# Kernel optimization log

Hardware: AMD Instinct MI355X
Metric: run time of the kernel (lower is better)

## Reference

```python
import jax, jax.numpy as jnp
import numpy as np

B, T, E, NH, NLEV = 16, 2048, 1024, 16, 12
HD = E // NH


def _level_matrix(length):
    # Vectorized version of get_level_index_weak (base=2): levels[t, s] for s < t.
    tt, ss = np.meshgrid(np.arange(length), np.arange(length), indexing='ij')
    t = tt.copy(); s = ss.copy()
    lev = np.zeros((length, length), dtype=np.int32)
    active = tt > ss
    while active.any():
        l = np.floor(np.log2(np.maximum(t, 1))).astype(np.int64)
        v = (1 << l)
        done = active & (s < v)
        lev[done] = (l[done] + 1).astype(np.int32)
        cont = active & ~done
        t = np.where(cont, t - v, t)
        s = np.where(cont, s - v, s)
        active = cont
    return lev  # lev[t,t] = 0 (diagonal uses level 0)


def setup_inputs() -> dict:
    key = jax.random.key(0)
    ks = jax.random.split(key, 12)
    s = 0.02
    inp = {
        'x': jax.random.normal(ks[0], (B, T, E), jnp.float32),
        'Wq': jax.random.normal(ks[1], (E, E), jnp.float32) * s,
        'bq': jnp.zeros((E,), jnp.float32),
        'Wk': jax.random.normal(ks[2], (E, E), jnp.float32) * s,
        'bk': jnp.zeros((E,), jnp.float32),
        'Wv': jax.random.normal(ks[3], (E, E), jnp.float32) * s,
        'bv': jnp.zeros((E,), jnp.float32),
        'A_log': jax.random.normal(ks[4], (T, NH), jnp.float32),
        'A_bias': jnp.zeros((T, NH), jnp.float32),
        'L': jax.random.normal(ks[5], (T, NH, NLEV), jnp.float32),
        'L_bias': jnp.zeros((T, NH, NLEV), jnp.float32),
        'Wo': jax.random.normal(ks[6], (E, E), jnp.float32) * s,
        'bo': jnp.zeros((E,), jnp.float32),
        'levels': jnp.asarray(_level_matrix(T)),
    }
    return inp


def reference(x, Wq, bq, Wk, bk, Wv, bv, A_log, A_bias, L, L_bias, Wo, bo, levels):
    Bn, Tn, En = x.shape
    NHh = A_log.shape[1]
    HDd = En // NHh
    # q/k projections exist in the original forward but are never used by the
    # hierarchical attention; keep only v (q/k are dead code -> omitted).
    v = (x @ Wv.T + bv).reshape(Bn, Tn, NHh, HDd).transpose(0, 2, 1, 3)  # [B,H,T,D]

    # Decay factors: prod(A[s+1:t+1]) == exp(cumsum(logA)[t] - cumsum(logA)[s]).
    A = jax.nn.sigmoid(A_log + A_bias)            # [T, H]
    cs = jnp.cumsum(jnp.log(A), axis=0)           # [T, H]
    decay = jnp.exp(cs[:, None, :] - cs[None, :, :])  # [t, s, H]; diag == 1

    # Hierarchical level weights: G[t, s, h] = (L + L_bias)[t, h, levels[t, s]].
    Le = L + L_bias                               # [T, H, NLEV]
    G = Le[jnp.arange(Tn)[:, None], :, levels]    # [t, s, H]

    causal = jnp.tril(jnp.ones((Tn, Tn), dtype=bool))[:, :, None]
    Hm = jnp.where(causal, G * decay, jnp.zeros((), x.dtype))  # [t, s, H]

    # Original softmaxes the full row (upper triangle is 0, not -inf) -> keep that.
    attn = jax.nn.softmax(Hm, axis=1)             # over source dim s
    out = jnp.einsum('tsh,bhsd->bhtd', attn, v)   # [B,H,T,D]
    out = out.transpose(0, 2, 1, 3).reshape(Bn, Tn, En)
    return out @ Wo.T + bo
```

## Files before the change

### kernel.cpp

```cpp
#include <hip/hip_runtime.h>
#include <stdint.h>

static constexpr int Bn = 16, Tn = 2048, En = 1024, NHn = 16, HDn = 64, NLEVn = 12;

typedef __attribute__((ext_vector_type(8))) short short8;
typedef __attribute__((ext_vector_type(4))) float floatx4;

__device__ __forceinline__ unsigned short f2bf(float f) {
  unsigned int u = __float_as_uint(f);
  u += 0x7fffu + ((u >> 16) & 1u);
  return (unsigned short)(u >> 16);
}
__device__ __forceinline__ float bf2f(unsigned short s) {
  return __uint_as_float(((unsigned int)s) << 16);
}

__device__ __forceinline__ void async16(const unsigned short* g, unsigned short* l) {
  __builtin_amdgcn_global_load_lds(
      (const __attribute__((address_space(1))) unsigned int*)g,
      (__attribute__((address_space(3))) unsigned int*)l, 16, 0, 0);
}

__global__ void k_cvt(const float* __restrict__ in, unsigned short* __restrict__ out, int n4) {
  int i = blockIdx.x * 256 + threadIdx.x;
  if (i < n4) {
    float4 v = ((const float4*)in)[i];
    ushort4 o;
    o.x = f2bf(v.x); o.y = f2bf(v.y); o.z = f2bf(v.z); o.w = f2bf(v.w);
    ((ushort4*)out)[i] = o;
  }
}

__global__ void k_scan(const float* __restrict__ A_log, const float* __restrict__ A_bias,
                       float* __restrict__ cs) {
  int h = blockIdx.x;
  int tid = threadIdx.x;
  __shared__ float part[256];
  float loc[8];
  float run = 0.f;
#pragma unroll
  for (int j = 0; j < 8; j++) {
    int t = tid * 8 + j;
    float x = A_log[t * NHn + h] + A_bias[t * NHn + h];
    float ls = -log1pf(__expf(-x));
    run += ls;
    loc[j] = run;
  }
  part[tid] = run;
  __syncthreads();
  for (int d = 1; d < 256; d <<= 1) {
    float v = (tid >= d) ? part[tid - d] : 0.f;
    __syncthreads();
    part[tid] += v;
    __syncthreads();
  }
  float off = (tid > 0) ? part[tid - 1] : 0.f;
#pragma unroll
  for (int j = 0; j < 8; j++) cs[(tid * 8 + j) * NHn + h] = loc[j] + off;
}

__global__ void k_weights(const float* __restrict__ L, const float* __restrict__ Lb,
                          const int* __restrict__ levels, const float* __restrict__ cs,
                          unsigned short* __restrict__ P, float* __restrict__ denom) {
  int t = blockIdx.x;
  int tid = threadIdx.x;
  __shared__ float Lrow[NHn * NLEVn];
  __shared__ float cst[NHn];
  __shared__ float dsum[NHn];
  if (tid < NHn * NLEVn) Lrow[tid] = L[t * NHn * NLEVn + tid] + Lb[t * NHn * NLEVn + tid];
  if (tid < NHn) { cst[tid] = cs[t * NHn + tid]; dsum[tid] = 0.f; }
  __syncthreads();
  float acc[NHn];
#pragma unroll
  for (int h = 0; h < NHn; h++) acc[h] = 0.f;
  for (int s = tid; s < Tn; s += 256) {
    int lev = levels[(size_t)t * Tn + s];
    bool causal = (s <= t);
    float csr[NHn];
    const float4* c4 = (const float4*)(cs + s * NHn);
#pragma unroll
    for (int q = 0; q < 4; q++) {
      float4 v = c4[q];
      csr[q * 4 + 0] = v.x; csr[q * 4 + 1] = v.y; csr[q * 4 + 2] = v.z; csr[q * 4 + 3] = v.w;
    }
#pragma unroll
    for (int h = 0; h < NHn; h++) {
      float w = 1.f;
      if (causal) {
        float dec = __expf(cst[h] - csr[h]);
        w = __expf(Lrow[h * NLEVn + lev] * dec);
      }
      unsigned short pb = f2bf(w);
      acc[h] += bf2f(pb);
      P[((size_t)h * Tn + t) * Tn + s] = pb;
    }
  }
  int lane = tid & 63;
#pragma unroll
  for (int h = 0; h < NHn; h++) {
    float v = acc[h];
    for (int o = 32; o > 0; o >>= 1) v += __shfl_down(v, o, 64);
    if (lane == 0) atomicAdd(&dsum[h], v);
  }
  __syncthreads();
  if (tid < NHn) denom[(size_t)tid * Tn + t] = dsum[tid];
}

__global__ __launch_bounds__(512)
void k_gemm_v(const unsigned short* __restrict__ A, const unsigned short* __restrict__ Bm,
              const float* __restrict__ bias, unsigned short* __restrict__ vt) {
  __shared__ unsigned short smem[24576];
  unsigned short* As = smem;
  unsigned short* Bs = smem + 16384;
  const int K = 1024;
  int tid = threadIdx.x;
  int wave = tid >> 6, lane = tid & 63;
  int wm = wave >> 1, wn = wave & 1;

  int flat = blockIdx.y * 8 + blockIdx.x;
  int xcd = flat & 7, slot = flat >> 3;
  int strip = xcd * 16 + (slot >> 3);
  int nt = slot & 7;
  int bm = strip * 256, bn = nt * 128;

  floatx4 zero4 = {0.f, 0.f, 0.f, 0.f};
  floatx4 acc[4][4];
#pragma unroll
  for (int i = 0; i < 4; i++)
#pragma unroll
    for (int j = 0; j < 4; j++) acc[i][j] = zero4;

  for (int k0 = 0; k0 < K; k0 += 64) {
    __syncthreads();
#pragma unroll
    for (int j = 0; j < 4; j++) {
      int f = j * 512 + tid;
      int r = f >> 3, c = f & 7;
      int cg = c ^ (r & 7);
      async16(&A[(size_t)(bm + r) * K + k0 + cg * 8], &As[f * 8]);
    }
#pragma unroll
    for (int j = 0; j < 2; j++) {
      int f = j * 512 + tid;
      int r = f >> 3, c = f & 7;
      int cg = c ^ (r & 7);
      async16(&Bm[(size_t)(bn + r) * K + k0 + cg * 8], &Bs[f * 8]);
    }
    __syncthreads();
#pragma unroll
    for (int kk = 0; kk < 2; kk++) {
      short8 af[4], bfr[4];
      int cgk = kk * 4 + (lane >> 4);
#pragma unroll
      for (int i = 0; i < 4; i++) {
        int m = wm * 64 + i * 16 + (lane & 15);
        af[i] = *(const short8*)&As[m * 64 + ((cgk ^ (m & 7)) * 8)];
        int n = wn * 64 + i * 16 + (lane & 15);
        bfr[i] = *(const short8*)&Bs[n * 64 + ((cgk ^ (n & 7)) * 8)];
      }
#pragma unroll
      for (int i = 0; i < 4; i++)
#pragma unroll
        for (int j = 0; j < 4; j++)
          acc[i][j] = __builtin_amdgcn_mfma_f32_16x16x32_bf16(af[i], bfr[j], acc[i][j], 0, 0, 0);
    }
  }

  int b = bm >> 11, t0 = bm & 2047;
  unsigned short* Ct = smem;
  const int S = 264;
#pragma unroll 1
  for (int pass = 0; pass < 2; pass++) {
    __syncthreads();
    if (wn == pass) {
#pragma unroll
      for (int i = 0; i < 4; i++) {
#pragma unroll
        for (int j = 0; j < 4; j++) {
          int colL = j * 16 + (lane & 15);
          float bia = bias[bn + pass * 64 + colL];
          int rowb = wm * 64 + i * 16 + (lane >> 4) * 4;
          ushort4 p;
          p.x = f2bf(acc[i][j][0] + bia);
          p.y = f2bf(acc[i][j][1] + bia);
          p.z = f2bf(acc[i][j][2] + bia);
          p.w = f2bf(acc[i][j][3] + bia);
          *(ushort4*)&Ct[colL * S + rowb] = p;
        }
      }
    }
    __syncthreads();
#pragma unroll
    for (int cc = 0; cc < 4; cc++) {
      int colL = wave * 8 + cc * 2 + (lane >> 5);
      int gc = bn + pass * 64 + colL;
      int h = gc >> 6, d = gc & 63;
      int tt = (lane & 31) * 8;
      short8 v = *(const short8*)&Ct[colL * S + tt];
      *(short8*)&vt[((size_t)((h * Bn + b) * HDn + d)) * Tn + t0 + tt] = v;
    }
  }
}


#define STAGE_A(kt, half, buf)                                                   \
  {                                                                              \
    _Pragma("unroll")                                                            \
    for (int j_ = 0; j_ < 2; j_++) {                                             \
      int f_ = j_ * 512 + tid;                                                   \
      int r_ = f_ >> 3, c_ = f_ & 7;                                             \
      int cg_ = c_ ^ (r_ & 7);                                                   \
      async16(&Ap[(size_t)(bm + (half) * 128 + r_) * K + (kt) * 64 + cg_ * 8],   \
              &smem[(buf) * 32768 + ((half) * 128 + r_) * 64 + c_ * 8]);         \
    }                                                                            \
  }

#define STAGE_B(kt, half, buf)                                                   \
  {                                                                              \
    _Pragma("unroll")                                                            \
    for (int j_ = 0; j_ < 2; j_++) {                                             \
      int f_ = j_ * 512 + tid;                                                   \
      int r_ = f_ >> 3, c_ = f_ & 7;                                             \
      int cg_ = c_ ^ (r_ & 7);                                                   \
      async16(&Bp[(size_t)(bn + (half) * 128 + r_) * K + (kt) * 64 + cg_ * 8],   \
              &smem[(buf) * 32768 + 16384 + ((half) * 128 + r_) * 64 + c_ * 8]); \
    }                                                                            \
  }

#define LOAD_A(buf, Mh)                                                          \
  {                                                                              \
    _Pragma("unroll")                                                            \
    for (int ii_ = 0; ii_ < 4; ii_++) {                                          \
      int m_ = (Mh) * 128 + wm * 64 + ii_ * 16 + (lane & 15);                    \
      _Pragma("unroll")                                                          \
      for (int kk_ = 0; kk_ < 2; kk_++) {                                        \
        int cgk_ = kk_ * 4 + (lane >> 4);                                        \
        aR[ii_][kk_] =                                                           \
            *(const short8*)&smem[(buf) * 32768 + m_ * 64 + ((cgk_ ^ (m_ & 7)) * 8)]; \
      }                                                                          \
    }                                                                            \
  }

#define LOAD_B(buf, Nh)                                                          \
  {                                                                              \
    _Pragma("unroll")                                                            \
    for (int jj_ = 0; jj_ < 2; jj_++) {                                          \
      int n_ = (Nh) * 128 + wn * 32 + jj_ * 16 + (lane & 15);                    \
      _Pragma("unroll")                                                          \
      for (int kk_ = 0; kk_ < 2; kk_++) {                                        \
        int cgk_ = kk_ * 4 + (lane >> 4);                                        \
        bR[jj_][kk_] = *(const short8*)&smem[(buf) * 32768 + 16384 + n_ * 64 +   \
                                             ((cgk_ ^ (n_ & 7)) * 8)];           \
      }                                                                          \
    }                                                                            \
  }

#define MFMA16(Mh, Nh)                                                           \
  {                                                                              \
    __builtin_amdgcn_s_setprio(1);                                               \
    _Pragma("unroll")                                                            \
    for (int kk_ = 0; kk_ < 2; kk_++)                                            \
      _Pragma("unroll")                                                          \
      for (int ii_ = 0; ii_ < 4; ii_++)                                          \
        _Pragma("unroll")                                                        \
        for (int jj_ = 0; jj_ < 2; jj_++)                                        \
          acc[(Mh) * 4 + ii_][(Nh) * 2 + jj_] = __builtin_amdgcn_mfma_f32_16x16x32_bf16( \
              aR[ii_][kk_], bR[jj_][kk_], acc[(Mh) * 4 + ii_][(Nh) * 2 + jj_], 0, 0, 0); \
    __builtin_amdgcn_s_setprio(0);                                               \
  }

#define WAIT4 asm volatile("s_waitcnt vmcnt(4)" ::: "memory")
#define LGKM8 asm volatile("s_waitcnt lgkmcnt(8)" ::: "memory")
#define BAR                                                                      \
  {                                                                              \
    asm volatile("" ::: "memory");                                               \
    __builtin_amdgcn_s_barrier();                                                \
    asm volatile("" ::: "memory");                                               \
  }

#define KTILE_BODY(buf, nbuf, tn)                                                \
  {                                                                              \
                                        \
    LOAD_A(buf, 0);                                                              \
    LOAD_B(buf, 0);                                                              \
    STAGE_A(tn, 0, nbuf);                                                        \
    LGKM8;                                                                       \
    WAIT4; BAR;                                                                  \
    MFMA16(0, 0);                                                                \
    BAR;                                                                         \
                                        \
    LOAD_B(buf, 1);                                                              \
    STAGE_B(tn, 0, nbuf);                                                        \
    WAIT4; BAR;                                                                  \
    MFMA16(0, 1);                                                                \
    BAR;                                                                         \
                                        \
    LOAD_A(buf, 1);                                                              \
    STAGE_B(tn, 1, nbuf);                                                        \
    WAIT4; BAR;                                                                  \
    MFMA16(1, 1);                                                                \
    BAR;                                                                         \
                           \
    LOAD_B(buf, 0);                                                              \
    STAGE_A(tn, 1, nbuf);                                                        \
    WAIT4; BAR;                                                                  \
    MFMA16(1, 0);                                                                \
    BAR;                                                                         \
  }

__global__ __launch_bounds__(512, 2)
void k_gemm_attn(const unsigned short* __restrict__ P, const unsigned short* __restrict__ vt,
                 const float* __restrict__ denom, unsigned short* __restrict__ outp) {
  __shared__ unsigned short smem[65536];
  const int K = Tn;
  int tid = threadIdx.x;
  int wave = tid >> 6, lane = tid & 63;
  int wm = wave >> 2, wn = wave & 3;

  int flat = blockIdx.y * 8 + blockIdx.x;
  int wg = (flat & 7) * 64 + (flat >> 3);
  int h = wg >> 5;
  int mt = (wg >> 2) & 7, nt = wg & 3;
  int bm = mt * 256, bn = nt * 256;

  const unsigned short* Ap = P + (size_t)h * Tn * Tn;
  const unsigned short* Bp = vt + (size_t)h * (Bn * HDn) * Tn;

  floatx4 zero4 = {0.f, 0.f, 0.f, 0.f};
  floatx4 acc[8][4];
#pragma unroll
  for (int i = 0; i < 8; i++)
#pragma unroll
    for (int j = 0; j < 4; j++) acc[i][j] = zero4;

  short8 aR[4][2], bR[2][2];

  STAGE_A(0, 0, 0);
  STAGE_B(0, 0, 0);
  STAGE_B(0, 1, 0);
  STAGE_A(0, 1, 0);
  WAIT4; BAR;

  const int nk = K / 64;
  for (int t = 0; t < nk; t++) {
    int buf = t & 1, nbuf = buf ^ 1;
    int tn = (t < nk - 1) ? t + 1 : nk - 1;
    KTILE_BODY(buf, nbuf, tn);
  }
  asm volatile("s_waitcnt vmcnt(0)" ::: "memory");

#pragma unroll
  for (int i = 0; i < 8; i++) {
    int rb = bm + (i >> 2) * 128 + wm * 64 + (i & 3) * 16 + (lane >> 4) * 4;
#pragma unroll
    for (int r = 0; r < 4; r++) {
      int row = rb + r;
      float sc = 1.f / denom[(size_t)h * Tn + row];
#pragma unroll
      for (int j = 0; j < 4; j++) {
        int col = bn + (j >> 1) * 128 + wn * 32 + (j & 1) * 16 + (lane & 15);
        int b = col >> 6, d = col & 63;
        outp[((size_t)(b * Tn + row)) * En + h * HDn + d] = f2bf(acc[i][j][r] * sc);
      }
    }
  }
}

__global__ __launch_bounds__(512, 2)
void k_gemm_out(const unsigned short* __restrict__ A, const unsigned short* __restrict__ Bm,
                const float* __restrict__ bias, float* __restrict__ out) {
  __shared__ unsigned short smem[65536];
  const int K = 1024, N = 1024;
  int tid = threadIdx.x;
  int wave = tid >> 6, lane = tid & 63;
  int wm = wave >> 2, wn = wave & 3;

  int flat = blockIdx.y * 8 + blockIdx.x;
  int wg = (flat & 7) * 64 + (flat >> 3);
  int mt = wg >> 2, nt = wg & 3;
  int bm = mt * 256, bn = nt * 256;

  const unsigned short* Ap = A;
  const unsigned short* Bp = Bm;

  floatx4 zero4 = {0.f, 0.f, 0.f, 0.f};
  floatx4 acc[8][4];
#pragma unroll
  for (int i = 0; i < 8; i++)
#pragma unroll
    for (int j = 0; j < 4; j++) acc[i][j] = zero4;

  short8 aR[4][2], bR[2][2];

  STAGE_A(0, 0, 0);
  STAGE_B(0, 0, 0);
  STAGE_B(0, 1, 0);
  STAGE_A(0, 1, 0);
  WAIT4; BAR;

  const int nk = K / 64;
  for (int t = 0; t < nk; t++) {
    int buf = t & 1, nbuf = buf ^ 1;
    int tn = (t < nk - 1) ? t + 1 : nk - 1;
    KTILE_BODY(buf, nbuf, tn);
  }
  asm volatile("s_waitcnt vmcnt(0)" ::: "memory");

#pragma unroll
  for (int i = 0; i < 8; i++) {
    int rb = bm + (i >> 2) * 128 + wm * 64 + (i & 3) * 16 + (lane >> 4) * 4;
#pragma unroll
    for (int r = 0; r < 4; r++) {
      int row = rb + r;
#pragma unroll
      for (int j = 0; j < 4; j++) {
        int col = bn + (j >> 1) * 128 + wn * 32 + (j & 1) * 16 + (lane & 15);
        out[(size_t)row * N + col] = acc[i][j][r] + bias[col];
      }
    }
  }
}

extern "C" void kernel_launch(void* const* d_in, const int* in_sizes, int n_in,
                              void* d_out, int out_size, void* d_ws, size_t ws_size,
                              hipStream_t stream) {
  const float* x      = (const float*)d_in[0];
  const float* Wv     = (const float*)d_in[5];
  const float* bv     = (const float*)d_in[6];
  const float* A_log  = (const float*)d_in[7];
  const float* A_bias = (const float*)d_in[8];
  const float* L      = (const float*)d_in[9];
  const float* Lb     = (const float*)d_in[10];
  const float* Wo     = (const float*)d_in[11];
  const float* bo     = (const float*)d_in[12];
  const int* levels   = (const int*)d_in[13];
  float* out = (float*)d_out;

  char* ws = (char*)d_ws;
  float* cs            = (float*)(ws + 0);
  float* denom         = (float*)(ws + 131072);
  unsigned short* Wvb  = (unsigned short*)(ws + 262144);
  unsigned short* Wob  = (unsigned short*)(ws + 2359296);
  unsigned short* xb   = (unsigned short*)(ws + 4456448);
  unsigned short* Pw   = (unsigned short*)(ws + 4456448);
  unsigned short* vt   = (unsigned short*)(ws + 138674176);
  unsigned short* outp = (unsigned short*)(ws + 205783040);
  if (ws_size < 272891904ULL) return;

  int nx4 = Bn * Tn * En / 4;
  k_cvt<<<(nx4 + 255) / 256, 256, 0, stream>>>(x, xb, nx4);
  int nw4 = En * En / 4;
  k_cvt<<<(nw4 + 255) / 256, 256, 0, stream>>>(Wv, Wvb, nw4);
  k_cvt<<<(nw4 + 255) / 256, 256, 0, stream>>>(Wo, Wob, nw4);
  k_scan<<<NHn, 256, 0, stream>>>(A_log, A_bias, cs);

  k_gemm_v<<<dim3(8, 128), 512, 0, stream>>>(xb, Wvb, bv, vt);

  k_weights<<<Tn, 256, 0, stream>>>(L, Lb, levels, cs, Pw, denom);

  k_gemm_attn<<<dim3(8, 64), 512, 0, stream>>>(Pw, vt, denom, outp);

  k_gemm_out<<<dim3(8, 64), 512, 0, stream>>>(outp, Wob, bo, out);
}
```

Baseline: 604.7 us.

## Rebuild V projection on pipelined 256x256 GEMM core and reorder staging waits

Replaces the simple synchronous V-projection GEMM (256x128 tiles, single-buffered) with the shared double-buffered 256x256 pipelined MFMA core used by the attention and output GEMMs, with a four-pass transposed epilogue. The per-quarter k-tile body is also reordered so each stage issues its next global-to-LDS load before waiting with vmcnt(6), replacing the earlier load-then-wait-vmcnt(4) and lgkmcnt pattern. The prologue barrier is dropped in all GEMMs. This aims to overlap memory with MFMA and raise tile reuse, at the risk of subtle ordering hazards in the new wait counts.

Result: slower. 664.3 us (+9.9%).

```diff
diff --git a/kernel.cpp b/kernel.cpp
--- a/kernel.cpp
+++ b/kernel.cpp
@@ -106,102 +106,6 @@
   if (tid < NHn) denom[(size_t)tid * Tn + t] = dsum[tid];
 }
 
-__global__ __launch_bounds__(512)
-void k_gemm_v(const unsigned short* __restrict__ A, const unsigned short* __restrict__ Bm,
-              const float* __restrict__ bias, unsigned short* __restrict__ vt) {
-  __shared__ unsigned short smem[24576];
-  unsigned short* As = smem;
-  unsigned short* Bs = smem + 16384;
-  const int K = 1024;
-  int tid = threadIdx.x;
-  int wave = tid >> 6, lane = tid & 63;
-  int wm = wave >> 1, wn = wave & 1;
-
-  int flat = blockIdx.y * 8 + blockIdx.x;
-  int xcd = flat & 7, slot = flat >> 3;
-  int strip = xcd * 16 + (slot >> 3);
-  int nt = slot & 7;
-  int bm = strip * 256, bn = nt * 128;
-
-  floatx4 zero4 = {0.f, 0.f, 0.f, 0.f};
-  floatx4 acc[4][4];
-#pragma unroll
-  for (int i = 0; i < 4; i++)
-#pragma unroll
-    for (int j = 0; j < 4; j++) acc[i][j] = zero4;
-
-  for (int k0 = 0; k0 < K; k0 += 64) {
-    __syncthreads();
-#pragma unroll
-    for (int j = 0; j < 4; j++) {
-      int f = j * 512 + tid;
-      int r = f >> 3, c = f & 7;
-      int cg = c ^ (r & 7);
-      async16(&A[(size_t)(bm + r) * K + k0 + cg * 8], &As[f * 8]);
-    }
-#pragma unroll
-    for (int j = 0; j < 2; j++) {
-      int f = j * 512 + tid;
-      int r = f >> 3, c = f & 7;
-      int cg = c ^ (r & 7);
-      async16(&Bm[(size_t)(bn + r) * K + k0 + cg * 8], &Bs[f * 8]);
-    }
-    __syncthreads();
-#pragma unroll
-    for (int kk = 0; kk < 2; kk++) {
-      short8 af[4], bfr[4];
-      int cgk = kk * 4 + (lane >> 4);
-#pragma unroll
-      for (int i = 0; i < 4; i++) {
-        int m = wm * 64 + i * 16 + (lane & 15);
-        af[i] = *(const short8*)&As[m * 64 + ((cgk ^ (m & 7)) * 8)];
-        int n = wn * 64 + i * 16 + (lane & 15);
-        bfr[i] = *(const short8*)&Bs[n * 64 + ((cgk ^ (n & 7)) * 8)];
-      }
-#pragma unroll
-      for (int i = 0; i < 4; i++)
-#pragma unroll
-        for (int j = 0; j < 4; j++)
-          acc[i][j] = __builtin_amdgcn_mfma_f32_16x16x32_bf16(af[i], bfr[j], acc[i][j], 0, 0, 0);
-    }
-  }
-
-  int b = bm >> 11, t0 = bm & 2047;
-  unsigned short* Ct = smem;
-  const int S = 264;
-#pragma unroll 1
-  for (int pass = 0; pass < 2; pass++) {
-    __syncthreads();
-    if (wn == pass) {
-#pragma unroll
-      for (int i = 0; i < 4; i++) {
-#pragma unroll
-        for (int j = 0; j < 4; j++) {
-          int colL = j * 16 + (lane & 15);
-          float bia = bias[bn + pass * 64 + colL];
-          int rowb = wm * 64 + i * 16 + (lane >> 4) * 4;
-          ushort4 p;
-          p.x = f2bf(acc[i][j][0] + bia);
-          p.y = f2bf(acc[i][j][1] + bia);
-          p.z = f2bf(acc[i][j][2] + bia);
-          p.w = f2bf(acc[i][j][3] + bia);
-          *(ushort4*)&Ct[colL * S + rowb] = p;
-        }
-      }
-    }
-    __syncthreads();
-#pragma unroll
-    for (int cc = 0; cc < 4; cc++) {
-      int colL = wave * 8 + cc * 2 + (lane >> 5);
-      int gc = bn + pass * 64 + colL;
-      int h = gc >> 6, d = gc & 63;
-      int tt = (lane & 31) * 8;
-      short8 v = *(const short8*)&Ct[colL * S + tt];
-      *(short8*)&vt[((size_t)((h * Bn + b) * HDn + d)) * Tn + t0 + tt] = v;
-    }
-  }
-}
-
 
 #define STAGE_A(kt, half, buf)                                                   \
   {                                                                              \
@@ -269,8 +173,7 @@
     __builtin_amdgcn_s_setprio(0);                                               \
   }
 
-#define WAIT4 asm volatile("s_waitcnt vmcnt(4)" ::: "memory")
-#define LGKM8 asm volatile("s_waitcnt lgkmcnt(8)" ::: "memory")
+#define WAIT6 asm volatile("s_waitcnt vmcnt(6)" ::: "memory")
 #define BAR                                                                      \
   {                                                                              \
     asm volatile("" ::: "memory");                                               \
@@ -280,33 +183,109 @@
 
 #define KTILE_BODY(buf, nbuf, tn)                                                \
   {                                                                              \
-                                        \
+                                  \
+    STAGE_A(tn, 0, nbuf);                                                        \
+    WAIT6; BAR;                                                                  \
     LOAD_A(buf, 0);                                                              \
     LOAD_B(buf, 0);                                                              \
-    STAGE_A(tn, 0, nbuf);                                                        \
-    LGKM8;                                                                       \
-    WAIT4; BAR;                                                                  \
     MFMA16(0, 0);                                                                \
     BAR;                                                                         \
-                                        \
+                               \
+    STAGE_B(tn, 0, nbuf);                                                        \
+    WAIT6; BAR;                                                                  \
     LOAD_B(buf, 1);                                                              \
-    STAGE_B(tn, 0, nbuf);                                                        \
-    WAIT4; BAR;                                                                  \
     MFMA16(0, 1);                                                                \
     BAR;                                                                         \
-                                        \
+                               \
+    STAGE_B(tn, 1, nbuf);                                                        \
+    WAIT6; BAR;                                                                  \
     LOAD_A(buf, 1);                                                              \
-    STAGE_B(tn, 1, nbuf);                                                        \
-    WAIT4; BAR;                                                                  \
     MFMA16(1, 1);                                                                \
     BAR;                                                                         \
-                           \
+                            \
+    STAGE_A(tn, 1, nbuf);                                                        \
+    WAIT6; BAR;                                                                  \
     LOAD_B(buf, 0);                                                              \
-    STAGE_A(tn, 1, nbuf);                                                        \
-    WAIT4; BAR;                                                                  \
     MFMA16(1, 0);                                                                \
     BAR;                                                                         \
   }
+
+__global__ __launch_bounds__(512, 2)
+void k_gemm_v(const unsigned short* __restrict__ A, const unsigned short* __restrict__ Bm,
+              const float* __restrict__ bias, unsigned short* __restrict__ vt) {
+  __shared__ unsigned short smem[65536];
+  const int K = 1024;
+  int tid = threadIdx.x;
+  int wave = tid >> 6, lane = tid & 63;
+  int wm = wave >> 2, wn = wave & 3;
+
+  int flat = blockIdx.y * 8 + blockIdx.x;
+  int wg = (flat & 7) * 64 + (flat >> 3);
+  int mt = wg >> 2, nt = wg & 3;
+  int bm = mt * 256, bn = nt * 256;
+
+  const unsigned short* Ap = A;
+  const unsigned short* Bp = Bm;
+
+  floatx4 zero4 = {0.f, 0.f, 0.f, 0.f};
+  floatx4 acc[8][4];
+#pragma unroll
+  for (int i = 0; i < 8; i++)
+#pragma unroll
+    for (int j = 0; j < 4; j++) acc[i][j] = zero4;
+
+  short8 aR[4][2], bR[2][2];
+
+  STAGE_A(0, 0, 0);
+  STAGE_B(0, 0, 0);
+  STAGE_B(0, 1, 0);
+  STAGE_A(0, 1, 0);
+
+  const int nk = K / 64;
+  for (int t = 0; t < nk; t++) {
+    int buf = t & 1, nbuf = buf ^ 1;
+    int tn = (t < nk - 1) ? t + 1 : nk - 1;
+    KTILE_BODY(buf, nbuf, tn);
+  }
+  asm volatile("s_waitcnt vmcnt(0)" ::: "memory");
+
+  int b = bm >> 11, t0 = bm & 2047;
+  unsigned short* Ct = smem;
+  const int S = 264;
+#pragma unroll 1
+  for (int pass = 0; pass < 4; pass++) {
+    __syncthreads();
+    if ((wn >> 1) == (pass & 1)) {
+      int jbase = (pass >> 1) * 2;
+#pragma unroll
+      for (int i = 0; i < 8; i++) {
+#pragma unroll
+        for (int jj = 0; jj < 2; jj++) {
+          int j = jbase + jj;
+          int colL = (wn & 1) * 32 + jj * 16 + (lane & 15);
+          float bia = bias[bn + pass * 64 + colL];
+          int rowb = (i >> 2) * 128 + wm * 64 + (i & 3) * 16 + (lane >> 4) * 4;
+          ushort4 p;
+          p.x = f2bf(acc[i][j][0] + bia);
+          p.y = f2bf(acc[i][j][1] + bia);
+          p.z = f2bf(acc[i][j][2] + bia);
+          p.w = f2bf(acc[i][j][3] + bia);
+          *(ushort4*)&Ct[colL * S + rowb] = p;
+        }
+      }
+    }
+    __syncthreads();
+#pragma unroll
+    for (int cc = 0; cc < 4; cc++) {
+      int colL = wave * 8 + cc * 2 + (lane >> 5);
+      int gc = bn + pass * 64 + colL;
+      int h = gc >> 6, d = gc & 63;
+      int tt = (lane & 31) * 8;
+      short8 v = *(const short8*)&Ct[colL * S + tt];
+      *(short8*)&vt[((size_t)((h * Bn + b) * HDn + d)) * Tn + t0 + tt] = v;
+    }
+  }
+}
 
 __global__ __launch_bounds__(512, 2)
 void k_gemm_attn(const unsigned short* __restrict__ P, const unsigned short* __restrict__ vt,
@@ -339,7 +318,6 @@
   STAGE_B(0, 0, 0);
   STAGE_B(0, 1, 0);
   STAGE_A(0, 1, 0);
-  WAIT4; BAR;
 
   const int nk = K / 64;
   for (int t = 0; t < nk; t++) {
@@ -396,7 +374,6 @@
   STAGE_B(0, 0, 0);
   STAGE_B(0, 1, 0);
   STAGE_A(0, 1, 0);
-  WAIT4; BAR;
 
   const int nk = K / 64;
   for (int t = 0; t < nk; t++) {
@@ -454,7 +431,7 @@
   k_cvt<<<(nw4 + 255) / 256, 256, 0, stream>>>(Wo, Wob, nw4);
   k_scan<<<NHn, 256, 0, stream>>>(A_log, A_bias, cs);
 
-  k_gemm_v<<<dim3(8, 128), 512, 0, stream>>>(xb, Wvb, bv, vt);
+  k_gemm_v<<<dim3(8, 64), 512, 0, stream>>>(xb, Wvb, bv, vt);
 
   k_weights<<<Tn, 256, 0, stream>>>(L, Lb, levels, cs, Pw, denom);
 
```

## Vectorize weight-row stores and reorder GEMM stage/wait schedule

Applied to the files above, without the earlier changes.

k_weights now has each thread handle 8 contiguous source positions. It loads their levels as int4 pairs and writes P as one 16-byte short8 per head, replacing strided 2-byte stores, which should give coalesced wide writes. In both GEMM kernels the k-tile body now issues the next global-to-LDS stage before waiting, using vmcnt(6) plus a barrier, then reads LDS fragments and runs the MFMAs. The prologue wait is dropped. This deepens the number of async loads in flight but changes the synchronisation ordering, so correctness depends on the vmcnt counts matching the number of loads per stage.

After: 637.2 us. 5.4% more time.

```diff
diff --git a/kernel.cpp b/kernel.cpp
--- a/kernel.cpp
+++ b/kernel.cpp
@@ -70,14 +70,23 @@
   if (tid < NHn * NLEVn) Lrow[tid] = L[t * NHn * NLEVn + tid] + Lb[t * NHn * NLEVn + tid];
   if (tid < NHn) { cst[tid] = cs[t * NHn + tid]; dsum[tid] = 0.f; }
   __syncthreads();
+
+  int s0 = tid * 8;
+  int4 lv0 = *(const int4*)&levels[(size_t)t * Tn + s0];
+  int4 lv1 = *(const int4*)&levels[(size_t)t * Tn + s0 + 4];
+  int lev[8] = {lv0.x, lv0.y, lv0.z, lv0.w, lv1.x, lv1.y, lv1.z, lv1.w};
+
   float acc[NHn];
 #pragma unroll
   for (int h = 0; h < NHn; h++) acc[h] = 0.f;
-  for (int s = tid; s < Tn; s += 256) {
-    int lev = levels[(size_t)t * Tn + s];
+  short8 pbv[NHn];
+
+#pragma unroll
+  for (int j = 0; j < 8; j++) {
+    int s = s0 + j;
     bool causal = (s <= t);
     float csr[NHn];
-    const float4* c4 = (const float4*)(cs + s * NHn);
+    const float4* c4 = (const float4*)(cs + (size_t)s * NHn);
 #pragma unroll
     for (int q = 0; q < 4; q++) {
       float4 v = c4[q];
@@ -88,13 +97,17 @@
       float w = 1.f;
       if (causal) {
         float dec = __expf(cst[h] - csr[h]);
-        w = __expf(Lrow[h * NLEVn + lev] * dec);
+        w = __expf(Lrow[h * NLEVn + lev[j]] * dec);
       }
       unsigned short pb = f2bf(w);
       acc[h] += bf2f(pb);
-      P[((size_t)h * Tn + t) * Tn + s] = pb;
-    }
-  }
+      pbv[h][j] = (short)pb;
+    }
+  }
+#pragma unroll
+  for (int h = 0; h < NHn; h++)
+    *(short8*)&P[((size_t)h * Tn + t) * Tn + s0] = pbv[h];
+
   int lane = tid & 63;
 #pragma unroll
   for (int h = 0; h < NHn; h++) {
@@ -269,8 +282,7 @@
     __builtin_amdgcn_s_setprio(0);                                               \
   }
 
-#define WAIT4 asm volatile("s_waitcnt vmcnt(4)" ::: "memory")
-#define LGKM8 asm volatile("s_waitcnt lgkmcnt(8)" ::: "memory")
+#define WAIT6 asm volatile("s_waitcnt vmcnt(6)" ::: "memory")
 #define BAR                                                                      \
   {                                                                              \
     asm volatile("" ::: "memory");                                               \
@@ -280,30 +292,29 @@
 
 #define KTILE_BODY(buf, nbuf, tn)                                                \
   {                                                                              \
-                                        \
+                                  \
+    STAGE_A(tn, 0, nbuf);                                                        \
+    WAIT6; BAR;                                                                  \
     LOAD_A(buf, 0);                                                              \
     LOAD_B(buf, 0);                                                              \
-    STAGE_A(tn, 0, nbuf);                                                        \
-    LGKM8;                                                                       \
-    WAIT4; BAR;                                                                  \
     MFMA16(0, 0);                                                                \
     BAR;                                                                         \
-                                        \
+                               \
+    STAGE_B(tn, 0, nbuf);                                                        \
+    WAIT6; BAR;                                                                  \
     LOAD_B(buf, 1);                                                              \
-    STAGE_B(tn, 0, nbuf);                                                        \
-    WAIT4; BAR;                                                                  \
     MFMA16(0, 1);                                                                \
     BAR;                                                                         \
-                                        \
+                               \
+    STAGE_B(tn, 1, nbuf);                                                        \
+    WAIT6; BAR;                                                                  \
     LOAD_A(buf, 1);                                                              \
-    STAGE_B(tn, 1, nbuf);                                                        \
-    WAIT4; BAR;                                                                  \
     MFMA16(1, 1);                                                                \
     BAR;                                                                         \
-                           \
+                            \
+    STAGE_A(tn, 1, nbuf);                                                        \
+    WAIT6; BAR;                                                                  \
     LOAD_B(buf, 0);                                                              \
-    STAGE_A(tn, 1, nbuf);                                                        \
-    WAIT4; BAR;                                                                  \
     MFMA16(1, 0);                                                                \
     BAR;                                                                         \
   }
@@ -339,7 +350,6 @@
   STAGE_B(0, 0, 0);
   STAGE_B(0, 1, 0);
   STAGE_A(0, 1, 0);
-  WAIT4; BAR;
 
   const int nk = K / 64;
   for (int t = 0; t < nk; t++) {
@@ -396,7 +406,6 @@
   STAGE_B(0, 0, 0);
   STAGE_B(0, 1, 0);
   STAGE_A(0, 1, 0);
-  WAIT4; BAR;
 
   const int nk = K / 64;
   for (int t = 0; t < nk; t++) {
```
